# Kernel optimization log

Hardware: AMD Instinct MI355X
Metric: run time of the kernel (lower is better)

## Reference

```python
import jax, jax.numpy as jnp
import numpy as np


def setup_inputs() -> dict:
    key = jax.random.key(0)
    k0, k1, k2, k3 = jax.random.split(key, 4)
    T, H, I, E, K = 2048, 2048, 1408, 8, 2  # tokens, hidden, intermediate, experts, top-k
    hidden_states = jax.random.normal(k0, (T, H), dtype=jnp.float32)
    router_weight = jax.random.normal(k1, (H, E), dtype=jnp.float32) * 0.02
    gate_up_weight = jax.random.normal(k2, (E, H, 2 * I), dtype=jnp.float32) * 0.02
    down_weight = jax.random.normal(k3, (E, I, H), dtype=jnp.float32) * 0.02
    return {
        "hidden_states": hidden_states,
        "router_weight": router_weight,
        "gate_up_weight": gate_up_weight,
        "down_weight": down_weight,
        "top_k": K,
    }


def reference(hidden_states, router_weight, gate_up_weight, down_weight, top_k):
    # Router: logits -> softmax -> top-k -> renormalize ('normalization' path)
    router_logits = hidden_states @ router_weight                  # [T, E]
    router_weights = jax.nn.softmax(router_logits, axis=-1)       # [T, E]
    topk_w, topk_idx = jax.lax.top_k(router_weights, top_k)       # [T, K]
    topk_w = topk_w / jnp.sum(topk_w, axis=-1, keepdims=True)     # router_weights_topk_reduced

    T, H = hidden_states.shape
    I = down_weight.shape[1]

    # Grouped gate_up GEMM (dense-per-expert reference for the grouped GMM)
    gate_up = jnp.einsum('th,ehf->etf', hidden_states, gate_up_weight)  # [E, T, 2I]
    gate, up = gate_up[..., :I], gate_up[..., I:]
    swish_out = jax.nn.silu(gate) * up                              # SWIGLU  [E, T, I]
    mlp_out = jnp.einsum('eti,eih->eth', swish_out, down_weight)    # [E, T, H]

    # Scatter-combine: gather each token's top-k expert outputs, weighted sum
    sel = mlp_out[topk_idx, jnp.arange(T)[:, None]]                 # [T, K, H]
    out = jnp.sum(sel * topk_w[..., None], axis=1)                  # [T, H]
    return out
```

## Files before the change

kernel.cpp:

```cpp
#include <hip/hip_runtime.h>
#include <hip/hip_bf16.h>
#include <math.h>

#define T_TOK 2048
#define HDIM  2048
#define IDIM  1408
#define NG    2816
#define NEXP  8
#define NPAIR (T_TOK*2)
#define RPAD  5120

typedef __attribute__((ext_vector_type(4))) float  f32x4;
typedef __attribute__((ext_vector_type(4))) short  s16x4;
typedef __attribute__((ext_vector_type(8))) short  s16x8;
typedef __attribute__((ext_vector_type(8))) __bf16 bf16x8;

__device__ __forceinline__ short f2bf(float f) {
  union { float f; unsigned u; } v; v.f = f;
  unsigned r = v.u + 0x7FFFu + ((v.u >> 16) & 1u);
  return (short)(r >> 16);
}

__device__ __forceinline__ float bf2f(short s) {
  union { unsigned u; float f; } v; v.u = ((unsigned)(unsigned short)s) << 16;
  return v.f;
}

__device__ __forceinline__ void gload_lds16(const void* g, void* l) {
  __builtin_amdgcn_global_load_lds((const __attribute__((address_space(1))) unsigned int*)g,
                                   (__attribute__((address_space(3))) unsigned int*)l,
                                   16, 0, 0);
}

__device__ __forceinline__ void grid_remap(int orig, int NB, int* nb, int* rblk) {
  int wgid = (orig & 7) * (NB * 5) + (orig >> 3);
  int cid = wgid / (NB * 5), c = wgid % (NB * 5);
  int nbg = c / 10, rem = c % 10;
  *rblk = (rem >> 1) * 8 + cid;
  *nb = nbg * 2 + (rem & 1);
}

__global__ void router_kernel(const float* __restrict__ hs, const float* __restrict__ rw,
                              int* __restrict__ pair_e, float* __restrict__ pair_w,
                              int* __restrict__ pair_pos, int* __restrict__ counts) {
  int wid = threadIdx.x >> 6, lane = threadIdx.x & 63;
  int t = blockIdx.x * 4 + wid;
  float acc[NEXP];
#pragma unroll
  for (int e = 0; e < NEXP; e++) acc[e] = 0.f;
  const float* h = hs + (size_t)t * HDIM;
  for (int k = lane; k < HDIM; k += 64) {
    float x = h[k];
    f32x4 w0 = *(const f32x4*)(rw + (size_t)k * NEXP);
    f32x4 w1 = *(const f32x4*)(rw + (size_t)k * NEXP + 4);
#pragma unroll
    for (int e = 0; e < 4; e++) { acc[e] += x * w0[e]; acc[e + 4] += x * w1[e]; }
  }
#pragma unroll
  for (int e = 0; e < NEXP; e++)
#pragma unroll
    for (int off = 32; off > 0; off >>= 1)
      acc[e] += __shfl_xor(acc[e], off, 64);
  if (lane == 0) {
    int i1 = 0; float v1 = acc[0];
#pragma unroll
    for (int e = 1; e < NEXP; e++) if (acc[e] > v1) { v1 = acc[e]; i1 = e; }
    int i2 = -1; float v2 = -3.4e38f;
#pragma unroll
    for (int e = 0; e < NEXP; e++) if (e != i1 && acc[e] > v2) { v2 = acc[e]; i2 = e; }
    float w2 = 1.f / (1.f + expf(v1 - v2));
    float w1 = 1.f - w2;
    int p1 = atomicAdd(&counts[i1], 1);
    int p2 = atomicAdd(&counts[i2], 1);
    pair_e[2*t]   = i1; pair_w[2*t]   = w1; pair_pos[2*t]   = p1;
    pair_e[2*t+1] = i2; pair_w[2*t+1] = w2; pair_pos[2*t+1] = p2;
  }
}

__global__ void prefix_kernel(const int* __restrict__ counts, int* __restrict__ offs) {
  if (threadIdx.x == 0) {
    int s = 0;
    for (int e = 0; e < NEXP; e++) { offs[e] = s; s += (counts[e] + 127) & ~127; }
    offs[NEXP] = s;
  }
}

__global__ void rowmap_kernel(const int* __restrict__ pair_e, const float* __restrict__ pair_w,
                              const int* __restrict__ pair_pos, const int* __restrict__ offs,
                              int* __restrict__ row_token, float* __restrict__ row_weight,
                              int* __restrict__ tok2row) {
  int p = blockIdx.x * 256 + threadIdx.x;
  if (p >= NPAIR) return;
  int e = pair_e[p];
  int row = offs[e] + pair_pos[p];
  row_token[row] = p >> 1;
  row_weight[row] = pair_w[p];
  tok2row[p] = row;
}

__global__ __launch_bounds__(256) void gather_kernel(const float* __restrict__ hs,
                                                     const int* __restrict__ row_token,
                                                     short* __restrict__ A_c) {
  int r = blockIdx.x;
  int tok = row_token[r];
  int t = threadIdx.x;
  if (tok < 0) {
    *(s16x8*)&A_c[(size_t)r * HDIM + t * 8] = (s16x8)0;
    return;
  }
  const float* src = hs + (size_t)tok * HDIM + t * 8;
  f32x4 v0 = *(const f32x4*)src;
  f32x4 v1 = *(const f32x4*)(src + 4);
  s16x8 o;
#pragma unroll
  for (int j = 0; j < 4; j++) { o[j] = f2bf(v0[j]); o[4 + j] = f2bf(v1[j]); }
  int dstg = (t & ~7) | ((t & 7) ^ (r & 7));
  *(s16x8*)&A_c[(size_t)r * HDIM + dstg * 8] = o;
}

__global__ __launch_bounds__(256) void convert_w_kernel(
    const float* __restrict__ src, short* __restrict__ dst, int K, int N, int e_base) {
  int e = blockIdx.z + e_base;
  src += (size_t)e * K * N;
  dst += (size_t)blockIdx.z * K * N;
  int n0 = blockIdx.x * 64, k0 = blockIdx.y * 64;
  __shared__ short tile[64 * 76];
  int tid = threadIdx.x;
#pragma unroll
  for (int it = 0; it < 4; it++) {
    int s = tid + it * 256;
    int kk = s >> 4, nn = (s & 15) * 4;
    f32x4 v = *(const f32x4*)(src + (size_t)(k0 + kk) * N + n0 + nn);
    s16x4 b;
#pragma unroll
    for (int j = 0; j < 4; j++) b[j] = f2bf(v[j]);
    *(s16x4*)&tile[kk * 76 + nn] = b;
  }
  __syncthreads();
#pragma unroll
  for (int it = 0; it < 2; it++) {
    int s = tid + it * 256;
    int n = s >> 3, g = s & 7;
    int gs = g ^ (n & 7);
    s16x8 o;
#pragma unroll
    for (int j = 0; j < 8; j++) o[j] = tile[(gs * 8 + j) * 76 + n];
    *(s16x8*)&dst[(size_t)(n0 + n) * K + k0 + g * 8] = o;
  }
}

__global__ __launch_bounds__(256) void gateup_kernel(
    const short* __restrict__ A_c, const short* __restrict__ W,
    const int* __restrict__ offs, short* __restrict__ S,
    int e_only, size_t w_e_stride) {
  int orig = blockIdx.y * gridDim.x + blockIdx.x;
  int nb, rblk;
  grid_remap(orig, 22, &nb, &rblk);
  int rb = rblk * 128;
  if (rb >= offs[NEXP]) return;
  int e = 0;
#pragma unroll
  for (int i = 1; i < NEXP; i++) e += (rb >= offs[i]);
  if (e_only >= 0 && e != e_only) return;
  const short* Wb = W + (e_only >= 0 ? 0 : (size_t)e * w_e_stride);
  const short* Ar = A_c + (size_t)rb * HDIM;
  const short* Bg = Wb + (size_t)(nb * 64) * HDIM;
  const short* Bu = Wb + (size_t)(IDIM + nb * 64) * HDIM;

  __shared__ short As[2][128 * 64];
  __shared__ short Bgs[2][64 * 64];
  __shared__ short Bus[2][64 * 64];
  int tid = threadIdx.x, lane = tid & 63, wid = tid >> 6;
  int wm = wid >> 1, wn = wid & 1;
  int lm = lane & 15, lg = lane >> 4;

  f32x4 accg[4][2], accu[4][2];
#pragma unroll
  for (int a = 0; a < 4; a++)
#pragma unroll
    for (int b = 0; b < 2; b++) { accg[a][b] = (f32x4)0.f; accu[a][b] = (f32x4)0.f; }

  auto STAGE = [&](int buf, int kt) {
    int k0 = kt * 64;
#pragma unroll
    for (int it = 0; it < 4; it++) {
      int idx = tid + it * 256;
      gload_lds16(Ar + (size_t)(idx >> 3) * HDIM + k0 + (idx & 7) * 8, &As[buf][idx * 8]);
    }
#pragma unroll
    for (int it = 0; it < 2; it++) {
      int idx = tid + it * 256;
      gload_lds16(Bg + (size_t)(idx >> 3) * HDIM + k0 + (idx & 7) * 8, &Bgs[buf][idx * 8]);
      gload_lds16(Bu + (size_t)(idx >> 3) * HDIM + k0 + (idx & 7) * 8, &Bus[buf][idx * 8]);
    }
  };

  STAGE(0, 0);
  int cur = 0;
  const int NT = HDIM / 64;
  for (int kt = 0; kt < NT; kt++) {
    if (kt + 1 < NT) {
      STAGE(cur ^ 1, kt + 1);
      asm volatile("s_waitcnt vmcnt(8)" ::: "memory");
    } else {
      asm volatile("s_waitcnt vmcnt(0)" ::: "memory");
    }
    __builtin_amdgcn_s_barrier();
    asm volatile("" ::: "memory");
#pragma unroll
    for (int ks = 0; ks < 2; ks++) {
      bf16x8 a[4], bg[2], bu[2];
#pragma unroll
      for (int mi = 0; mi < 4; mi++) {
        int m = wm * 64 + mi * 16 + lm;
        a[mi] = *(const bf16x8*)&As[cur][m * 64 + (((ks * 4 + lg) ^ (m & 7)) * 8)];
      }
#pragma unroll
      for (int nf = 0; nf < 2; nf++) {
        int n = wn * 32 + nf * 16 + lm;
        int off = n * 64 + (((ks * 4 + lg) ^ (n & 7)) * 8);
        bg[nf] = *(const bf16x8*)&Bgs[cur][off];
        bu[nf] = *(const bf16x8*)&Bus[cur][off];
      }
#pragma unroll
      for (int mi = 0; mi < 4; mi++)
#pragma unroll
        for (int nf = 0; nf < 2; nf++) {
          accg[mi][nf] = __builtin_amdgcn_mfma_f32_16x16x32_bf16(a[mi], bg[nf], accg[mi][nf], 0, 0, 0);
          accu[mi][nf] = __builtin_amdgcn_mfma_f32_16x16x32_bf16(a[mi], bu[nf], accu[mi][nf], 0, 0, 0);
        }
    }
    asm volatile("" ::: "memory");
    __builtin_amdgcn_s_barrier();
    cur ^= 1;
  }
#pragma unroll
  for (int mi = 0; mi < 4; mi++)
#pragma unroll
    for (int nf = 0; nf < 2; nf++)
#pragma unroll
      for (int j = 0; j < 4; j++) {
        int row = wm * 64 + mi * 16 + lg * 4 + j;
        int rg = rb + row;
        int c6 = wn * 32 + nf * 16 + lm;
        int dc = (((c6 >> 3) ^ (rg & 7)) << 3) | (c6 & 7);
        float g = accg[mi][nf][j], u = accu[mi][nf][j];
        float sv = (g / (1.f + expf(-g))) * u;
        S[(size_t)rg * IDIM + nb * 64 + dc] = f2bf(sv);
      }
}

__global__ __launch_bounds__(256) void down_kernel(
    const short* __restrict__ S, const short* __restrict__ W,
    const int* __restrict__ offs, short* __restrict__ Sout,
    int e_only, size_t w_e_stride) {
  int orig = blockIdx.y * gridDim.x + blockIdx.x;
  int nb, rblk;
  grid_remap(orig, 16, &nb, &rblk);
  int rb = rblk * 128;
  if (rb >= offs[NEXP]) return;
  int e = 0;
#pragma unroll
  for (int i = 1; i < NEXP; i++) e += (rb >= offs[i]);
  if (e_only >= 0 && e != e_only) return;
  const short* Ar = S + (size_t)rb * IDIM;
  const short* Bw = W + (e_only >= 0 ? 0 : (size_t)e * w_e_stride) + (size_t)(nb * 128) * IDIM;

  __shared__ short As[2][128 * 64];
  __shared__ short Bs[2][128 * 64];
  int tid = threadIdx.x, lane = tid & 63, wid = tid >> 6;
  int wm = wid >> 1, wn = wid & 1;
  int lm = lane & 15, lg = lane >> 4;

  f32x4 acc[4][4];
#pragma unroll
  for (int a = 0; a < 4; a++)
#pragma unroll
    for (int b = 0; b < 4; b++) acc[a][b] = (f32x4)0.f;

  auto STAGE = [&](int buf, int kt) {
    int k0 = kt * 64;
#pragma unroll
    for (int it = 0; it < 4; it++) {
      int idx = tid + it * 256;
      gload_lds16(Ar + (size_t)(idx >> 3) * IDIM + k0 + (idx & 7) * 8, &As[buf][idx * 8]);
      gload_lds16(Bw + (size_t)(idx >> 3) * IDIM + k0 + (idx & 7) * 8, &Bs[buf][idx * 8]);
    }
  };

  STAGE(0, 0);
  int cur = 0;
  const int NT = IDIM / 64;
  for (int kt = 0; kt < NT; kt++) {
    if (kt + 1 < NT) {
      STAGE(cur ^ 1, kt + 1);
      asm volatile("s_waitcnt vmcnt(8)" ::: "memory");
    } else {
      asm volatile("s_waitcnt vmcnt(0)" ::: "memory");
    }
    __builtin_amdgcn_s_barrier();
    asm volatile("" ::: "memory");
#pragma unroll
    for (int ks = 0; ks < 2; ks++) {
      bf16x8 a[4], b[4];
#pragma unroll
      for (int mi = 0; mi < 4; mi++) {
        int m = wm * 64 + mi * 16 + lm;
        a[mi] = *(const bf16x8*)&As[cur][m * 64 + (((ks * 4 + lg) ^ (m & 7)) * 8)];
      }
#pragma unroll
      for (int nf = 0; nf < 4; nf++) {
        int n = wn * 64 + nf * 16 + lm;
        b[nf] = *(const bf16x8*)&Bs[cur][n * 64 + (((ks * 4 + lg) ^ (n & 7)) * 8)];
      }
#pragma unroll
      for (int mi = 0; mi < 4; mi++)
#pragma unroll
        for (int nf = 0; nf < 4; nf++)
          acc[mi][nf] = __builtin_amdgcn_mfma_f32_16x16x32_bf16(a[mi], b[nf], acc[mi][nf], 0, 0, 0);
    }
    asm volatile("" ::: "memory");
    __builtin_amdgcn_s_barrier();
    cur ^= 1;
  }
#pragma unroll
  for (int mi = 0; mi < 4; mi++)
#pragma unroll
    for (int j = 0; j < 4; j++) {
      int row = wm * 64 + mi * 16 + lg * 4 + j;
#pragma unroll
      for (int nf = 0; nf < 4; nf++) {
        int col = nb * 128 + wn * 64 + nf * 16 + lm;
        Sout[(size_t)(rb + row) * HDIM + col] = f2bf(acc[mi][nf][j]);
      }
    }
}

__global__ __launch_bounds__(256) void combine_kernel(
    const short* __restrict__ Sout, const int* __restrict__ tok2row,
    const float* __restrict__ row_weight, float* __restrict__ out) {
  int t = blockIdx.x;
  int r1 = tok2row[2 * t], r2 = tok2row[2 * t + 1];
  float w1 = row_weight[r1], w2 = row_weight[r2];
  int c = threadIdx.x * 8;
  s16x8 a = *(const s16x8*)&Sout[(size_t)r1 * HDIM + c];
  s16x8 b = *(const s16x8*)&Sout[(size_t)r2 * HDIM + c];
  float* o = out + (size_t)t * HDIM + c;
#pragma unroll
  for (int j = 0; j < 8; j++) o[j] = w1 * bf2f(a[j]) + w2 * bf2f(b[j]);
}

extern "C" void kernel_launch(void* const* d_in, const int* in_sizes, int n_in,
                              void* d_out, int out_size, void* d_ws, size_t ws_size,
                              hipStream_t stream) {
  const float* hs  = (const float*)d_in[0];
  const float* rw  = (const float*)d_in[1];
  const float* guw = (const float*)d_in[2];
  const float* dw  = (const float*)d_in[3];
  float* out = (float*)d_out;

  char* ws = (char*)d_ws;
  size_t off = 0;
  auto take = [&](size_t b) { size_t p = off; off = (off + b + 255) & ~(size_t)255; return p; };
  size_t s_off      = take((size_t)RPAD * IDIM * 2);
  int*   counts     = (int*)(ws + take(32 * 4));
  int*   offs       = (int*)(ws + take(16 * 4));
  int*   pair_e     = (int*)(ws + take(NPAIR * 4));
  float* pair_w     = (float*)(ws + take(NPAIR * 4));
  int*   pair_pos   = (int*)(ws + take(NPAIR * 4));
  int*   row_token  = (int*)(ws + take(RPAD * 4));
  float* row_weight = (float*)(ws + take(RPAD * 4));
  int*   tok2row    = (int*)(ws + take(NPAIR * 4));
  size_t ac_off  = take((size_t)RPAD * HDIM * 2);
  size_t wg_off  = off;

  short* S   = (short*)(ws + s_off);
  short* A_c = (short*)(ws + ac_off);

  const size_t WG_BYTES = (size_t)NEXP * NG * HDIM * 2;
  const size_t WD_BYTES = (size_t)NEXP * HDIM * IDIM * 2;
  bool full = ws_size >= wg_off + WG_BYTES;

  hipMemsetAsync(counts, 0, 32 * 4, stream);
  hipMemsetAsync(row_token, 0xFF, RPAD * 4, stream);

  router_kernel<<<T_TOK / 4, 256, 0, stream>>>(hs, rw, pair_e, pair_w, pair_pos, counts);
  prefix_kernel<<<1, 64, 0, stream>>>(counts, offs);
  rowmap_kernel<<<NPAIR / 256, 256, 0, stream>>>(pair_e, pair_w, pair_pos, offs,
                                                 row_token, row_weight, tok2row);
  gather_kernel<<<RPAD, 256, 0, stream>>>(hs, row_token, A_c);

  if (full) {
    short* Wg   = (short*)(ws + wg_off);
    short* Wd   = (short*)(ws + ac_off);
    short* Sout = (short*)(ws + ac_off + ((size_t)48 << 20));
    convert_w_kernel<<<dim3(NG / 64, HDIM / 64, NEXP), 256, 0, stream>>>(guw, Wg, HDIM, NG, 0);
    gateup_kernel<<<dim3(22, 40, 1), 256, 0, stream>>>(A_c, Wg, offs, S, -1, (size_t)NG * HDIM);
    convert_w_kernel<<<dim3(HDIM / 64, IDIM / 64, NEXP), 256, 0, stream>>>(dw, Wd, IDIM, HDIM, 0);
    down_kernel<<<dim3(16, 40, 1), 256, 0, stream>>>(S, Wd, offs, Sout, -1, (size_t)HDIM * IDIM);
    combine_kernel<<<T_TOK, 256, 0, stream>>>(Sout, tok2row, row_weight, out);
  } else {
    short* slot = (short*)(ws + wg_off);
    short* Sout = (short*)(ws + wg_off + ((size_t)12 << 20));
    (void)WD_BYTES;
    for (int e = 0; e < NEXP; e++) {
      convert_w_kernel<<<dim3(NG / 64, HDIM / 64, 1), 256, 0, stream>>>(guw, slot, HDIM, NG, e);
      gateup_kernel<<<dim3(22, 40, 1), 256, 0, stream>>>(A_c, slot, offs, S, e, 0);
    }
    for (int e = 0; e < NEXP; e++) {
      convert_w_kernel<<<dim3(HDIM / 64, IDIM / 64, 1), 256, 0, stream>>>(dw, slot, IDIM, HDIM, e);
      down_kernel<<<dim3(16, 40, 1), 256, 0, stream>>>(S, slot, offs, Sout, e, 0);
    }
    combine_kernel<<<T_TOK, 256, 0, stream>>>(Sout, tok2row, row_weight, out);
  }
}
```

Measured before the change: 310.8 us.

## Enlarge grouped GEMM tiles to 256 rows with 512-thread blocks and phased MFMA schedule

Both grouped GEMMs move from 128-row tiles with 256 threads to 256x256 (down) and 256x(2x128) (gate/up) tiles run by 512 threads. Expert padding grows to 256 rows to match, and the grid becomes 1D with a new XCD-aware remap. The k-loop is split into four barrier-separated phases with sched_barrier and setprio around the MFMA bursts. Larger tiles raise data reuse per LDS load, but padding waste grows, fewer workgroups cover the 256 CUs, and LDS use reaches 128KB per block. Workspace aliasing is also changed so the converted down weights reuse the gate/up weight buffer and Sout reuses the gathered-activation buffer.

```diff
diff --git a/kernel.cpp b/kernel.cpp
--- a/kernel.cpp
+++ b/kernel.cpp
@@ -8,7 +8,7 @@
 #define NG    2816
 #define NEXP  8
 #define NPAIR (T_TOK*2)
-#define RPAD  5120
+#define RPAD  6144
 
 typedef __attribute__((ext_vector_type(4))) float  f32x4;
 typedef __attribute__((ext_vector_type(4))) short  s16x4;
@@ -30,14 +30,6 @@
   __builtin_amdgcn_global_load_lds((const __attribute__((address_space(1))) unsigned int*)g,
                                    (__attribute__((address_space(3))) unsigned int*)l,
                                    16, 0, 0);
-}
-
-__device__ __forceinline__ void grid_remap(int orig, int NB, int* nb, int* rblk) {
-  int wgid = (orig & 7) * (NB * 5) + (orig >> 3);
-  int cid = wgid / (NB * 5), c = wgid % (NB * 5);
-  int nbg = c / 10, rem = c % 10;
-  *rblk = (rem >> 1) * 8 + cid;
-  *nb = nbg * 2 + (rem & 1);
 }
 
 __global__ void router_kernel(const float* __restrict__ hs, const float* __restrict__ rw,
@@ -80,7 +72,7 @@
 __global__ void prefix_kernel(const int* __restrict__ counts, int* __restrict__ offs) {
   if (threadIdx.x == 0) {
     int s = 0;
-    for (int e = 0; e < NEXP; e++) { offs[e] = s; s += (counts[e] + 127) & ~127; }
+    for (int e = 0; e < NEXP; e++) { offs[e] = s; s += (counts[e] + 255) & ~255; }
     offs[NEXP] = s;
   }
 }
@@ -149,14 +141,14 @@
   }
 }
 
-__global__ __launch_bounds__(256) void gateup_kernel(
+__global__ __launch_bounds__(512, 2) void gateup_kernel(
     const short* __restrict__ A_c, const short* __restrict__ W,
     const int* __restrict__ offs, short* __restrict__ S,
     int e_only, size_t w_e_stride) {
-  int orig = blockIdx.y * gridDim.x + blockIdx.x;
-  int nb, rblk;
-  grid_remap(orig, 22, &nb, &rblk);
-  int rb = rblk * 128;
+  int orig = blockIdx.x;
+  int wgid = (orig & 7) * 33 + (orig >> 3);
+  int rblk = wgid / 11, nb = wgid % 11;
+  int rb = rblk * 256;
   if (rb >= offs[NEXP]) return;
   int e = 0;
 #pragma unroll
@@ -164,117 +156,122 @@
   if (e_only >= 0 && e != e_only) return;
   const short* Wb = W + (e_only >= 0 ? 0 : (size_t)e * w_e_stride);
   const short* Ar = A_c + (size_t)rb * HDIM;
-  const short* Bg = Wb + (size_t)(nb * 64) * HDIM;
-  const short* Bu = Wb + (size_t)(IDIM + nb * 64) * HDIM;
-
-  __shared__ short As[2][128 * 64];
-  __shared__ short Bgs[2][64 * 64];
-  __shared__ short Bus[2][64 * 64];
+  const short* Bg = Wb + (size_t)(nb * 128) * HDIM;
+  const short* Bu = Wb + (size_t)(IDIM + nb * 128) * HDIM;
+
+  __shared__ short As[2][256 * 64];
+  __shared__ short Bs[2][256 * 64];
   int tid = threadIdx.x, lane = tid & 63, wid = tid >> 6;
-  int wm = wid >> 1, wn = wid & 1;
+  int wm = wid >> 2, wn = wid & 3;
   int lm = lane & 15, lg = lane >> 4;
 
-  f32x4 accg[4][2], accu[4][2];
-#pragma unroll
-  for (int a = 0; a < 4; a++)
-#pragma unroll
-    for (int b = 0; b < 2; b++) { accg[a][b] = (f32x4)0.f; accu[a][b] = (f32x4)0.f; }
+  f32x4 acc[8][4];
+#pragma unroll
+  for (int a = 0; a < 8; a++)
+#pragma unroll
+    for (int b = 0; b < 4; b++) acc[a][b] = (f32x4)0.f;
 
   auto STAGE = [&](int buf, int kt) {
     int k0 = kt * 64;
 #pragma unroll
     for (int it = 0; it < 4; it++) {
-      int idx = tid + it * 256;
+      int idx = tid + it * 512;
       gload_lds16(Ar + (size_t)(idx >> 3) * HDIM + k0 + (idx & 7) * 8, &As[buf][idx * 8]);
     }
 #pragma unroll
     for (int it = 0; it < 2; it++) {
-      int idx = tid + it * 256;
-      gload_lds16(Bg + (size_t)(idx >> 3) * HDIM + k0 + (idx & 7) * 8, &Bgs[buf][idx * 8]);
-      gload_lds16(Bu + (size_t)(idx >> 3) * HDIM + k0 + (idx & 7) * 8, &Bus[buf][idx * 8]);
+      int idx = tid + it * 512;
+      gload_lds16(Bg + (size_t)(idx >> 3) * HDIM + k0 + (idx & 7) * 8, &Bs[buf][idx * 8]);
+      gload_lds16(Bu + (size_t)(idx >> 3) * HDIM + k0 + (idx & 7) * 8, &Bs[buf][8192 + idx * 8]);
     }
   };
 
   STAGE(0, 0);
-  int cur = 0;
   const int NT = HDIM / 64;
+  bf16x8 bq[4];
+#pragma unroll 1
   for (int kt = 0; kt < NT; kt++) {
-    if (kt + 1 < NT) {
-      STAGE(cur ^ 1, kt + 1);
-      asm volatile("s_waitcnt vmcnt(8)" ::: "memory");
-    } else {
-      asm volatile("s_waitcnt vmcnt(0)" ::: "memory");
-    }
-    __builtin_amdgcn_s_barrier();
-    asm volatile("" ::: "memory");
-#pragma unroll
-    for (int ks = 0; ks < 2; ks++) {
-      bf16x8 a[4], bg[2], bu[2];
-#pragma unroll
-      for (int mi = 0; mi < 4; mi++) {
-        int m = wm * 64 + mi * 16 + lm;
-        a[mi] = *(const bf16x8*)&As[cur][m * 64 + (((ks * 4 + lg) ^ (m & 7)) * 8)];
-      }
-#pragma unroll
-      for (int nf = 0; nf < 2; nf++) {
-        int n = wn * 32 + nf * 16 + lm;
-        int off = n * 64 + (((ks * 4 + lg) ^ (n & 7)) * 8);
-        bg[nf] = *(const bf16x8*)&Bgs[cur][off];
-        bu[nf] = *(const bf16x8*)&Bus[cur][off];
-      }
-#pragma unroll
-      for (int mi = 0; mi < 4; mi++)
-#pragma unroll
-        for (int nf = 0; nf < 2; nf++) {
-          accg[mi][nf] = __builtin_amdgcn_mfma_f32_16x16x32_bf16(a[mi], bg[nf], accg[mi][nf], 0, 0, 0);
-          accu[mi][nf] = __builtin_amdgcn_mfma_f32_16x16x32_bf16(a[mi], bu[nf], accu[mi][nf], 0, 0, 0);
+    int cur = kt & 1;
+#pragma unroll
+    for (int p = 0; p < 4; p++) {
+      if (p == 0) {
+        if (kt + 1 < NT) {
+          STAGE(cur ^ 1, kt + 1);
+          asm volatile("s_waitcnt vmcnt(8)" ::: "memory");
+        } else {
+          asm volatile("s_waitcnt vmcnt(0)" ::: "memory");
         }
-    }
-    asm volatile("" ::: "memory");
-    __builtin_amdgcn_s_barrier();
-    cur ^= 1;
-  }
-#pragma unroll
-  for (int mi = 0; mi < 4; mi++)
-#pragma unroll
-    for (int nf = 0; nf < 2; nf++)
+      }
+      __builtin_amdgcn_s_barrier();
+      __builtin_amdgcn_sched_barrier(0);
+      const int ks = p >> 1, mih = p & 1;
+      bf16x8 av[4];
+#pragma unroll
+      for (int mi4 = 0; mi4 < 4; mi4++) {
+        int m = wm * 128 + (mih * 4 + mi4) * 16 + lm;
+        av[mi4] = *(const bf16x8*)&As[cur][m * 64 + (((ks * 4 + lg) ^ (m & 7)) * 8)];
+      }
+      if (mih == 0) {
+#pragma unroll
+        for (int nf = 0; nf < 4; nf++) {
+          int rbq = (nf >> 1) * 128 + wn * 32 + (nf & 1) * 16 + lm;
+          bq[nf] = *(const bf16x8*)&Bs[cur][rbq * 64 + (((ks * 4 + lg) ^ (rbq & 7)) * 8)];
+        }
+      }
+      __builtin_amdgcn_s_setprio(1);
+#pragma unroll
+      for (int mi4 = 0; mi4 < 4; mi4++)
+#pragma unroll
+        for (int nf = 0; nf < 4; nf++)
+          acc[mih * 4 + mi4][nf] =
+              __builtin_amdgcn_mfma_f32_16x16x32_bf16(av[mi4], bq[nf], acc[mih * 4 + mi4][nf], 0, 0, 0);
+      __builtin_amdgcn_s_setprio(0);
+      __builtin_amdgcn_sched_barrier(0);
+      __builtin_amdgcn_s_barrier();
+    }
+  }
+#pragma unroll
+  for (int mi = 0; mi < 8; mi++)
+#pragma unroll
+    for (int nfg = 0; nfg < 2; nfg++)
 #pragma unroll
       for (int j = 0; j < 4; j++) {
-        int row = wm * 64 + mi * 16 + lg * 4 + j;
+        int row = wm * 128 + mi * 16 + lg * 4 + j;
         int rg = rb + row;
-        int c6 = wn * 32 + nf * 16 + lm;
-        int dc = (((c6 >> 3) ^ (rg & 7)) << 3) | (c6 & 7);
-        float g = accg[mi][nf][j], u = accu[mi][nf][j];
+        int scol = nb * 128 + wn * 32 + nfg * 16 + lm;
+        int base = scol & ~63, o = scol & 63;
+        int dc = (((o >> 3) ^ (rg & 7)) << 3) | (o & 7);
+        float g = acc[mi][nfg][j], u = acc[mi][nfg + 2][j];
         float sv = (g / (1.f + expf(-g))) * u;
-        S[(size_t)rg * IDIM + nb * 64 + dc] = f2bf(sv);
-      }
-}
-
-__global__ __launch_bounds__(256) void down_kernel(
+        S[(size_t)rg * IDIM + base + dc] = f2bf(sv);
+      }
+}
+
+__global__ __launch_bounds__(512, 2) void down_kernel(
     const short* __restrict__ S, const short* __restrict__ W,
     const int* __restrict__ offs, short* __restrict__ Sout,
     int e_only, size_t w_e_stride) {
-  int orig = blockIdx.y * gridDim.x + blockIdx.x;
-  int nb, rblk;
-  grid_remap(orig, 16, &nb, &rblk);
-  int rb = rblk * 128;
+  int orig = blockIdx.x;
+  int wgid = (orig & 7) * 24 + (orig >> 3);
+  int rblk = wgid / 8, nb = wgid % 8;
+  int rb = rblk * 256;
   if (rb >= offs[NEXP]) return;
   int e = 0;
 #pragma unroll
   for (int i = 1; i < NEXP; i++) e += (rb >= offs[i]);
   if (e_only >= 0 && e != e_only) return;
   const short* Ar = S + (size_t)rb * IDIM;
-  const short* Bw = W + (e_only >= 0 ? 0 : (size_t)e * w_e_stride) + (size_t)(nb * 128) * IDIM;
-
-  __shared__ short As[2][128 * 64];
-  __shared__ short Bs[2][128 * 64];
+  const short* Bw = W + (e_only >= 0 ? 0 : (size_t)e * w_e_stride) + (size_t)(nb * 256) * IDIM;
+
+  __shared__ short As[2][256 * 64];
+  __shared__ short Bs[2][256 * 64];
   int tid = threadIdx.x, lane = tid & 63, wid = tid >> 6;
-  int wm = wid >> 1, wn = wid & 1;
+  int wm = wid >> 2, wn = wid & 3;
   int lm = lane & 15, lg = lane >> 4;
 
-  f32x4 acc[4][4];
-#pragma unroll
-  for (int a = 0; a < 4; a++)
+  f32x4 acc[8][4];
+#pragma unroll
+  for (int a = 0; a < 8; a++)
 #pragma unroll
     for (int b = 0; b < 4; b++) acc[a][b] = (f32x4)0.f;
 
@@ -282,58 +279,66 @@
     int k0 = kt * 64;
 #pragma unroll
     for (int it = 0; it < 4; it++) {
-      int idx = tid + it * 256;
+      int idx = tid + it * 512;
       gload_lds16(Ar + (size_t)(idx >> 3) * IDIM + k0 + (idx & 7) * 8, &As[buf][idx * 8]);
       gload_lds16(Bw + (size_t)(idx >> 3) * IDIM + k0 + (idx & 7) * 8, &Bs[buf][idx * 8]);
     }
   };
 
   STAGE(0, 0);
-  int cur = 0;
   const int NT = IDIM / 64;
+  bf16x8 bq[4];
+#pragma unroll 1
   for (int kt = 0; kt < NT; kt++) {
-    if (kt + 1 < NT) {
-      STAGE(cur ^ 1, kt + 1);
-      asm volatile("s_waitcnt vmcnt(8)" ::: "memory");
-    } else {
-      asm volatile("s_waitcnt vmcnt(0)" ::: "memory");
-    }
-    __builtin_amdgcn_s_barrier();
-    asm volatile("" ::: "memory");
-#pragma unroll
-    for (int ks = 0; ks < 2; ks++) {
-      bf16x8 a[4], b[4];
-#pragma unroll
-      for (int mi = 0; mi < 4; mi++) {
-        int m = wm * 64 + mi * 16 + lm;
-        a[mi] = *(const bf16x8*)&As[cur][m * 64 + (((ks * 4 + lg) ^ (m & 7)) * 8)];
-      }
-#pragma unroll
-      for (int nf = 0; nf < 4; nf++) {
-        int n = wn * 64 + nf * 16 + lm;
-        b[nf] = *(const bf16x8*)&Bs[cur][n * 64 + (((ks * 4 + lg) ^ (n & 7)) * 8)];
-      }
-#pragma unroll
-      for (int mi = 0; mi < 4; mi++)
+    int cur = kt & 1;
+#pragma unroll
+    for (int p = 0; p < 4; p++) {
+      if (p == 0) {
+        if (kt + 1 < NT) {
+          STAGE(cur ^ 1, kt + 1);
+          asm volatile("s_waitcnt vmcnt(8)" ::: "memory");
+        } else {
+          asm volatile("s_waitcnt vmcnt(0)" ::: "memory");
+        }
+      }
+      __builtin_amdgcn_s_barrier();
+      __builtin_amdgcn_sched_barrier(0);
+      const int ks = p >> 1, mih = p & 1;
+      bf16x8 av[4];
+#pragma unroll
+      for (int mi4 = 0; mi4 < 4; mi4++) {
+        int m = wm * 128 + (mih * 4 + mi4) * 16 + lm;
+        av[mi4] = *(const bf16x8*)&As[cur][m * 64 + (((ks * 4 + lg) ^ (m & 7)) * 8)];
+      }
+      if (mih == 0) {
+#pragma unroll
+        for (int nf = 0; nf < 4; nf++) {
+          int rbq = wn * 64 + nf * 16 + lm;
+          bq[nf] = *(const bf16x8*)&Bs[cur][rbq * 64 + (((ks * 4 + lg) ^ (rbq & 7)) * 8)];
+        }
+      }
+      __builtin_amdgcn_s_setprio(1);
+#pragma unroll
+      for (int mi4 = 0; mi4 < 4; mi4++)
 #pragma unroll
         for (int nf = 0; nf < 4; nf++)
-          acc[mi][nf] = __builtin_amdgcn_mfma_f32_16x16x32_bf16(a[mi], b[nf], acc[mi][nf], 0, 0, 0);
-    }
-    asm volatile("" ::: "memory");
-    __builtin_amdgcn_s_barrier();
-    cur ^= 1;
-  }
-#pragma unroll
-  for (int mi = 0; mi < 4; mi++)
-#pragma unroll
-    for (int j = 0; j < 4; j++) {
-      int row = wm * 64 + mi * 16 + lg * 4 + j;
-#pragma unroll
-      for (int nf = 0; nf < 4; nf++) {
-        int col = nb * 128 + wn * 64 + nf * 16 + lm;
+          acc[mih * 4 + mi4][nf] =
+              __builtin_amdgcn_mfma_f32_16x16x32_bf16(av[mi4], bq[nf], acc[mih * 4 + mi4][nf], 0, 0, 0);
+      __builtin_amdgcn_s_setprio(0);
+      __builtin_amdgcn_sched_barrier(0);
+      __builtin_amdgcn_s_barrier();
+    }
+  }
+#pragma unroll
+  for (int mi = 0; mi < 8; mi++)
+#pragma unroll
+    for (int nf = 0; nf < 4; nf++)
+#pragma unroll
+      for (int j = 0; j < 4; j++) {
+        int row = wm * 128 + mi * 16 + lg * 4 + j;
+        int col = nb * 256 + wn * 64 + nf * 16 + lm;
         Sout[(size_t)(rb + row) * HDIM + col] = f2bf(acc[mi][nf][j]);
       }
-    }
 }
 
 __global__ __launch_bounds__(256) void combine_kernel(
@@ -374,11 +379,11 @@
   size_t ac_off  = take((size_t)RPAD * HDIM * 2);
   size_t wg_off  = off;
 
-  short* S   = (short*)(ws + s_off);
-  short* A_c = (short*)(ws + ac_off);
+  short* S    = (short*)(ws + s_off);
+  short* A_c  = (short*)(ws + ac_off);
+  short* Sout = (short*)(ws + ac_off);
 
   const size_t WG_BYTES = (size_t)NEXP * NG * HDIM * 2;
-  const size_t WD_BYTES = (size_t)NEXP * HDIM * IDIM * 2;
   bool full = ws_size >= wg_off + WG_BYTES;
 
   hipMemsetAsync(counts, 0, 32 * 4, stream);
@@ -391,25 +396,22 @@
   gather_kernel<<<RPAD, 256, 0, stream>>>(hs, row_token, A_c);
 
   if (full) {
-    short* Wg   = (short*)(ws + wg_off);
-    short* Wd   = (short*)(ws + ac_off);
-    short* Sout = (short*)(ws + ac_off + ((size_t)48 << 20));
+    short* Wg = (short*)(ws + wg_off);
+    short* Wd = (short*)(ws + wg_off);
     convert_w_kernel<<<dim3(NG / 64, HDIM / 64, NEXP), 256, 0, stream>>>(guw, Wg, HDIM, NG, 0);
-    gateup_kernel<<<dim3(22, 40, 1), 256, 0, stream>>>(A_c, Wg, offs, S, -1, (size_t)NG * HDIM);
+    gateup_kernel<<<264, 512, 0, stream>>>(A_c, Wg, offs, S, -1, (size_t)NG * HDIM);
     convert_w_kernel<<<dim3(HDIM / 64, IDIM / 64, NEXP), 256, 0, stream>>>(dw, Wd, IDIM, HDIM, 0);
-    down_kernel<<<dim3(16, 40, 1), 256, 0, stream>>>(S, Wd, offs, Sout, -1, (size_t)HDIM * IDIM);
+    down_kernel<<<192, 512, 0, stream>>>(S, Wd, offs, Sout, -1, (size_t)HDIM * IDIM);
     combine_kernel<<<T_TOK, 256, 0, stream>>>(Sout, tok2row, row_weight, out);
   } else {
     short* slot = (short*)(ws + wg_off);
-    short* Sout = (short*)(ws + wg_off + ((size_t)12 << 20));
-    (void)WD_BYTES;
     for (int e = 0; e < NEXP; e++) {
       convert_w_kernel<<<dim3(NG / 64, HDIM / 64, 1), 256, 0, stream>>>(guw, slot, HDIM, NG, e);
-      gateup_kernel<<<dim3(22, 40, 1), 256, 0, stream>>>(A_c, slot, offs, S, e, 0);
+      gateup_kernel<<<264, 512, 0, stream>>>(A_c, slot, offs, S, e, 0);
     }
     for (int e = 0; e < NEXP; e++) {
       convert_w_kernel<<<dim3(HDIM / 64, IDIM / 64, 1), 256, 0, stream>>>(dw, slot, IDIM, HDIM, e);
-      down_kernel<<<dim3(16, 40, 1), 256, 0, stream>>>(S, slot, offs, Sout, e, 0);
+      down_kernel<<<192, 512, 0, stream>>>(S, slot, offs, Sout, e, 0);
     }
     combine_kernel<<<T_TOK, 256, 0, stream>>>(Sout, tok2row, row_weight, out);
   }
```

Measured after the change: 363.3 us. 1.17x slower.
